# Performance work log

Measured on AMD Instinct MI355X. Metric: run time of the kernel, lower is better.

The kernel has to match this reference:

```python
import jax, jax.numpy as jnp
import numpy as np

B, S, D, E, H = 4, 2048, 1024, 8, 2048


def setup_inputs() -> dict:
    key = jax.random.key(0)
    ks = jax.random.split(key, 8)
    s_in = 1.0 / np.sqrt(D)   # torch Linear default init scale (uniform bound)
    s_hid = 1.0 / np.sqrt(H)
    return {
        "x": jax.random.normal(ks[0], (B, S, D), dtype=jnp.float32),
        "W1": jax.random.uniform(ks[1], (E, D, H), minval=-s_in, maxval=s_in, dtype=jnp.float32),
        "b1": jax.random.uniform(ks[2], (E, H), minval=-s_in, maxval=s_in, dtype=jnp.float32),
        "W2": jax.random.uniform(ks[3], (E, H, D), minval=-s_hid, maxval=s_hid, dtype=jnp.float32),
        "b2": jax.random.uniform(ks[4], (E, D), minval=-s_hid, maxval=s_hid, dtype=jnp.float32),
        "Wg": jax.random.uniform(ks[5], (D, E), minval=-s_in, maxval=s_in, dtype=jnp.float32),
        "bg": jax.random.uniform(ks[6], (E,), minval=-s_in, maxval=s_in, dtype=jnp.float32),
    }


def reference(x, W1, b1, W2, b2, Wg, bg):
    # All-experts dense MoE (eval mode: dropout is identity).
    # hidden: [B,S,E,H]
    h = jax.nn.relu(jnp.einsum("bsd,edh->bseh", x, W1) + b1)
    # expert outputs: [B,S,E,D]
    expert_out = jnp.einsum("bseh,ehd->bsed", h, W2) + b2
    # gate (raw linear, no softmax in original): [B,S,E]
    gate = jnp.einsum("bsd,de->bse", x, Wg) + bg
    # gate-weighted sum over experts -> [B,S,D]
    return jnp.einsum("bse,bsed->bsd", gate, expert_out)
```

## Files before the change

### kernel.cpp

```cpp
#include <hip/hip_runtime.h>

#define NTOK 8192
#define DDIM 1024
#define HDIM 2048
#define NEXP 8
#define GEXP 2
#define G1_NKT 16
#define G2_NKT 64

typedef unsigned short u16;
typedef short bf16x8 __attribute__((ext_vector_type(8)));
typedef float f32x4 __attribute__((ext_vector_type(4)));
typedef float float4_t __attribute__((ext_vector_type(4)));

__device__ __forceinline__ u16 f2bf(float f) {
  unsigned u = __float_as_uint(f);
  u += 0x7FFFu + ((u >> 16) & 1u);
  return (u16)(u >> 16);
}

#define GLOAD_LDS16(gp, lp)                                                     \
  __builtin_amdgcn_global_load_lds(                                             \
      (const __attribute__((address_space(1))) unsigned int*)(gp),              \
      (__attribute__((address_space(3))) unsigned int*)(lp), 16, 0, 0)

#define VMW(n) asm volatile("s_waitcnt vmcnt(" #n ")" ::: "memory")
#define ENTRYB()                                                                \
  { __builtin_amdgcn_s_barrier(); __builtin_amdgcn_sched_barrier(0); }

__global__ void k_prep(const float* __restrict__ x, const float* __restrict__ Wg,
                       const float* __restrict__ bg,
                       u16* __restrict__ xb, float* __restrict__ gate) {
  const int tok = (blockIdx.x * 256 + threadIdx.x) >> 6;
  const int lane = threadIdx.x & 63;
  const float* xr = x + (size_t)tok * DDIM;
  u16* xo = xb + (size_t)tok * DDIM;
  float s[NEXP];
#pragma unroll
  for (int e = 0; e < NEXP; ++e) s[e] = 0.f;
#pragma unroll
  for (int it = 0; it < 2; ++it) {
    const int d0 = lane * 8 + it * 512;
    float4_t v0 = *(const float4_t*)(xr + d0);
    float4_t v1 = *(const float4_t*)(xr + d0 + 4);
    union { bf16x8 v; u16 h[8]; } u;
    u.h[0] = f2bf(v0.x); u.h[1] = f2bf(v0.y); u.h[2] = f2bf(v0.z); u.h[3] = f2bf(v0.w);
    u.h[4] = f2bf(v1.x); u.h[5] = f2bf(v1.y); u.h[6] = f2bf(v1.z); u.h[7] = f2bf(v1.w);
    *(bf16x8*)(xo + d0) = u.v;
    float xv[8] = {v0.x, v0.y, v0.z, v0.w, v1.x, v1.y, v1.z, v1.w};
#pragma unroll
    for (int j = 0; j < 8; ++j) {
      const float4_t w0 = *(const float4_t*)(Wg + (size_t)(d0 + j) * NEXP);
      const float4_t w1 = *(const float4_t*)(Wg + (size_t)(d0 + j) * NEXP + 4);
      s[0] += xv[j] * w0.x; s[1] += xv[j] * w0.y;
      s[2] += xv[j] * w0.z; s[3] += xv[j] * w0.w;
      s[4] += xv[j] * w1.x; s[5] += xv[j] * w1.y;
      s[6] += xv[j] * w1.z; s[7] += xv[j] * w1.w;
    }
  }
#pragma unroll
  for (int off = 32; off; off >>= 1)
#pragma unroll
    for (int e = 0; e < NEXP; ++e) s[e] += __shfl_down(s[e], off);
  if (lane == 0) {
#pragma unroll
    for (int e = 0; e < NEXP; ++e) gate[(size_t)tok * NEXP + e] = s[e] + bg[e];
  }
}

__global__ void k_transpose(const float* __restrict__ in, u16* __restrict__ out,
                            int R, int C, size_t oexp, int orstride) {
  __shared__ float t[64][65];
  const int rb = blockIdx.x * 64, cb = blockIdx.y * 64;
  const float* pin = in + (size_t)blockIdx.z * R * C;
  u16* pout = out + (size_t)blockIdx.z * oexp;
  const int tid = threadIdx.x;
  {
    const int r = tid >> 4;
    const int c4 = (tid & 15) * 4;
#pragma unroll
    for (int i = 0; i < 4; ++i) {
      float4_t v = *(const float4_t*)(pin + (size_t)(rb + r + 16 * i) * C + cb + c4);
      t[r + 16 * i][c4 + 0] = v.x;
      t[r + 16 * i][c4 + 1] = v.y;
      t[r + 16 * i][c4 + 2] = v.z;
      t[r + 16 * i][c4 + 3] = v.w;
    }
  }
  __syncthreads();
  {
    const int oc = tid >> 3;
    const int r8 = (tid & 7) * 8;
#pragma unroll
    for (int jp = 0; jp < 2; ++jp) {
      const int ocol = oc + 32 * jp;
      union { bf16x8 v; u16 h[8]; } u;
#pragma unroll
      for (int k = 0; k < 8; ++k) u.h[k] = f2bf(t[r8 + k][ocol]);
      *(bf16x8*)(pout + (size_t)(cb + ocol) * orstride + rb + r8) = u.v;
    }
  }
}

__global__ __launch_bounds__(512, 2) void k_g1(
    const u16* __restrict__ A, const u16* __restrict__ Bt,
    const float* __restrict__ bias, const float* __restrict__ gate,
    int ebase, u16* __restrict__ Cout) {
  __shared__ __align__(16) u16 lds[65536];
  const int tid = threadIdx.x, lane = tid & 63, wid = tid >> 6;
  const int wm = wid >> 2, wn = wid & 3;
  const int wg = blockIdx.x;
  const int xcd = wg & 7, lo = wg >> 3;
  const int tm = (xcd >> 1) * 8 + (lo >> 3);
  const int tn = (xcd & 1) * 8 + (lo & 7);
  const int bm = tm * 256, bn = tn * 256;

  const int srow = tid >> 3;
  const int scol = ((tid & 7) ^ (srow & 7)) << 3;
  const u16* gA = A + (size_t)(bm + srow) * 1024 + scol;
  const u16* gB = Bt + (size_t)(bn + srow) * 1024 + scol;
  const int dofs = wid * 512;

  u16* aB0 = lds;          u16* bB0 = lds + 16384;
  u16* aB1 = lds + 32768;  u16* bB1 = lds + 49152;

  const int fr = lane & 15, fq = lane >> 4, xr = fr & 7;
  const int so0 = ((0 + fq) ^ xr) << 3;
  const int so1 = ((4 + fq) ^ xr) << 3;

  f32x4 acc[4][4][2] = {};
  bf16x8 av[4][2], bv[2][2];

#define G1_SA(dst, hh, ts)                                                      \
  { GLOAD_LDS16(gA + (size_t)((hh)*128     ) * 1024 + (size_t)(ts) * 64,        \
                (dst) + ((hh)*128     ) * 64 + dofs);                           \
    GLOAD_LDS16(gA + (size_t)((hh)*128 + 64) * 1024 + (size_t)(ts) * 64,        \
                (dst) + ((hh)*128 + 64) * 64 + dofs); }
#define G1_SB(dst, hh, ts)                                                      \
  { GLOAD_LDS16(gB + (size_t)((hh)*128     ) * 1024 + (size_t)(ts) * 64,        \
                (dst) + ((hh)*128     ) * 64 + dofs);                           \
    GLOAD_LDS16(gB + (size_t)((hh)*128 + 64) * 1024 + (size_t)(ts) * 64,        \
                (dst) + ((hh)*128 + 64) * 64 + dofs); }
#define RD_A(src, MH)                                                           \
  { _Pragma("unroll") for (int i_ = 0; i_ < 4; ++i_) {                          \
      const int rb_ = ((MH)*128 + wm * 64 + i_ * 16 + fr) << 6;                 \
      av[i_][0] = *(const bf16x8*)((src) + rb_ + so0);                          \
      av[i_][1] = *(const bf16x8*)((src) + rb_ + so1); } }
#define RD_B(src, NH)                                                           \
  { _Pragma("unroll") for (int n_ = 0; n_ < 2; ++n_) {                          \
      const int rb_ = ((NH)*128 + wn * 32 + n_ * 16 + fr) << 6;                 \
      bv[n_][0] = *(const bf16x8*)((src) + rb_ + so0);                          \
      bv[n_][1] = *(const bf16x8*)((src) + rb_ + so1); } }
#define MMA16(Q)                                                                \
  { __builtin_amdgcn_s_setprio(1);                                              \
    _Pragma("unroll") for (int i_ = 0; i_ < 4; ++i_)                            \
    _Pragma("unroll") for (int n_ = 0; n_ < 2; ++n_) {                          \
      acc[Q][i_][n_] = __builtin_amdgcn_mfma_f32_16x16x32_bf16(                 \
          av[i_][0], bv[n_][0], acc[Q][i_][n_], 0, 0, 0);                       \
      acc[Q][i_][n_] = __builtin_amdgcn_mfma_f32_16x16x32_bf16(                 \
          av[i_][1], bv[n_][1], acc[Q][i_][n_], 0, 0, 0); }                     \
    __builtin_amdgcn_s_setprio(0); }

  G1_SA(aB0, 0, 0); G1_SB(bB0, 0, 0); G1_SA(aB0, 1, 0); G1_SB(bB0, 1, 0);

  u16 *aC_ = aB0, *bC_ = bB0, *aN_ = aB1, *bN_ = bB1;

#pragma unroll 1
  for (int t = 0; t < G1_NKT; ++t) {
    const bool s1 = (t + 1 < G1_NKT);
    VMW(4); ENTRYB();
    RD_A(aC_, 0); RD_B(bC_, 0);
    if (s1) G1_SA(aN_, 0, t + 1);
    MMA16(0);
    if (s1) { VMW(4); } else { VMW(2); }
    ENTRYB();
    RD_A(aC_, 1);
    if (s1) G1_SB(bN_, 0, t + 1);
    MMA16(2);
    if (s1) { VMW(4); } else { VMW(0); }
    ENTRYB();
    RD_B(bC_, 1);
    if (s1) G1_SA(aN_, 1, t + 1);
    MMA16(3);
    RD_A(aC_, 0);
    if (s1) G1_SB(bN_, 1, t + 1);
    MMA16(1);
    u16* tp;
    tp = aC_; aC_ = aN_; aN_ = tp;
    tp = bC_; bC_ = bN_; bN_ = tp;
  }

#pragma unroll
  for (int q = 0; q < 4; ++q) {
    const int MH = q >> 1, NH = q & 1;
    const int cb0 = bn + NH * 128 + wn * 32;
    const int e = ebase + (cb0 >> 11);
    float bcol[2];
#pragma unroll
    for (int n = 0; n < 2; ++n) bcol[n] = bias[cb0 + n * 16 + fr];
#pragma unroll
    for (int i = 0; i < 4; ++i) {
#pragma unroll
      for (int j = 0; j < 4; ++j) {
        const int r = bm + MH * 128 + wm * 64 + i * 16 + fq * 4 + j;
        const float g = gate[(size_t)r * NEXP + e];
#pragma unroll
        for (int n = 0; n < 2; ++n) {
          float v = fmaxf(acc[q][i][n][j] + bcol[n], 0.f) * g;
          Cout[(size_t)r * (GEXP * HDIM) + cb0 + n * 16 + fr] = f2bf(v);
        }
      }
    }
  }
#undef G1_SA
#undef G1_SB
#undef RD_A
#undef RD_B
#undef MMA16
}

__global__ __launch_bounds__(512, 2) void k_g2(
    const u16* __restrict__ A, const u16* __restrict__ Bt,
    const float* __restrict__ bias, const float* __restrict__ gate,
    float* __restrict__ Cout, int accum) {
  __shared__ __align__(16) u16 lds[49152];
  const int tid = threadIdx.x, lane = tid & 63, wid = tid >> 6;
  const int wm = wid >> 2, wn = wid & 3;
  const int wg = blockIdx.x;
  const int xcd = wg & 7, lo = wg >> 3;
  const int tm = xcd * 8 + (lo >> 2);
  const int tn = lo & 3;
  const int bm = tm * 128, bn = tn * 256;

  const int srow = tid >> 3;
  const int scol = ((tid & 7) ^ (srow & 7)) << 3;
  const u16* gA = A + (size_t)(bm + srow) * (GEXP * HDIM) + scol;
  const u16* gB = Bt + (size_t)(bn + srow) * HDIM + scol;
  const int dofs = wid * 512;

  u16* aB0 = lds;          u16* bB0 = lds + 8192;
  u16* aB1 = lds + 24576;  u16* bB1 = lds + 32768;

  const int fr = lane & 15, fq = lane >> 4, xr = fr & 7;
  const int so0 = ((0 + fq) ^ xr) << 3;
  const int so1 = ((4 + fq) ^ xr) << 3;

  f32x4 acc[2][4][2] = {};
  bf16x8 av[4][2], bv[2][2];

#define G2_BOFF(ts) ((size_t)((ts) >> 5) * ((size_t)DDIM * HDIM) +              \
                     (size_t)((ts) & 31) * 64)
#define G2_SA(dst, ts)                                                          \
  { GLOAD_LDS16(gA + (size_t)(ts) * 64, (dst) + dofs);                          \
    GLOAD_LDS16(gA + (size_t)64 * (GEXP * HDIM) + (size_t)(ts) * 64,            \
                (dst) + 4096 + dofs); }
#define G2_SB(dst, hh, ts)                                                      \
  { GLOAD_LDS16(gB + (size_t)((hh)*128     ) * HDIM + G2_BOFF(ts),              \
                (dst) + ((hh)*128     ) * 64 + dofs);                           \
    GLOAD_LDS16(gB + (size_t)((hh)*128 + 64) * HDIM + G2_BOFF(ts),              \
                (dst) + ((hh)*128 + 64) * 64 + dofs); }
#define G2_RDA(src)                                                             \
  { _Pragma("unroll") for (int i_ = 0; i_ < 4; ++i_) {                          \
      const int rb_ = (wm * 64 + i_ * 16 + fr) << 6;                            \
      av[i_][0] = *(const bf16x8*)((src) + rb_ + so0);                          \
      av[i_][1] = *(const bf16x8*)((src) + rb_ + so1); } }
#define G2_RDB(src, NH)                                                         \
  { _Pragma("unroll") for (int n_ = 0; n_ < 2; ++n_) {                          \
      const int rb_ = ((NH)*128 + wn * 32 + n_ * 16 + fr) << 6;                 \
      bv[n_][0] = *(const bf16x8*)((src) + rb_ + so0);                          \
      bv[n_][1] = *(const bf16x8*)((src) + rb_ + so1); } }
#define G2_MMA(Q)                                                               \
  { __builtin_amdgcn_s_setprio(1);                                              \
    _Pragma("unroll") for (int i_ = 0; i_ < 4; ++i_)                            \
    _Pragma("unroll") for (int n_ = 0; n_ < 2; ++n_) {                          \
      acc[Q][i_][n_] = __builtin_amdgcn_mfma_f32_16x16x32_bf16(                 \
          av[i_][0], bv[n_][0], acc[Q][i_][n_], 0, 0, 0);                       \
      acc[Q][i_][n_] = __builtin_amdgcn_mfma_f32_16x16x32_bf16(                 \
          av[i_][1], bv[n_][1], acc[Q][i_][n_], 0, 0, 0); }                     \
    __builtin_amdgcn_s_setprio(0); }

  G2_SA(aB0, 0); G2_SB(bB0, 0, 0); G2_SB(bB0, 1, 0);

  u16 *aC_ = aB0, *bC_ = bB0, *aN_ = aB1, *bN_ = bB1;

#pragma unroll 1
  for (int t = 0; t < G2_NKT; ++t) {
    const bool s1 = (t + 1 < G2_NKT);
    VMW(2); ENTRYB();
    G2_RDA(aC_); G2_RDB(bC_, 0);
    if (s1) { G2_SA(aN_, t + 1); G2_SB(bN_, 0, t + 1); }
    G2_MMA(0);
    if (s1) { VMW(4); } else { VMW(0); }
    ENTRYB();
    G2_RDB(bC_, 1);
    if (s1) G2_SB(bN_, 1, t + 1);
    G2_MMA(1);
    u16* tp;
    tp = aC_; aC_ = aN_; aN_ = tp;
    tp = bC_; bC_ = bN_; bN_ = tp;
  }

  float b2c[2][2][NEXP];
  if (!accum) {
#pragma unroll
    for (int nh = 0; nh < 2; ++nh)
#pragma unroll
      for (int n = 0; n < 2; ++n)
#pragma unroll
        for (int e = 0; e < NEXP; ++e)
          b2c[nh][n][e] = bias[(size_t)e * DDIM + bn + nh * 128 + wn * 32 + n * 16 + fr];
  }
#pragma unroll
  for (int NH = 0; NH < 2; ++NH) {
    const int cb0 = bn + NH * 128 + wn * 32;
#pragma unroll
    for (int i = 0; i < 4; ++i) {
#pragma unroll
      for (int j = 0; j < 4; ++j) {
        const int r = bm + wm * 64 + i * 16 + fq * 4 + j;
        if (!accum) {
          float g8[NEXP];
#pragma unroll
          for (int e = 0; e < NEXP; ++e) g8[e] = gate[(size_t)r * NEXP + e];
#pragma unroll
          for (int n = 0; n < 2; ++n) {
            float v = acc[NH][i][n][j];
#pragma unroll
            for (int e = 0; e < NEXP; ++e) v += g8[e] * b2c[NH][n][e];
            Cout[(size_t)r * DDIM + cb0 + n * 16 + fr] = v;
          }
        } else {
#pragma unroll
          for (int n = 0; n < 2; ++n) {
            const size_t idx = (size_t)r * DDIM + cb0 + n * 16 + fr;
            Cout[idx] += acc[NH][i][n][j];
          }
        }
      }
    }
  }
#undef G2_BOFF
#undef G2_SA
#undef G2_SB
#undef G2_RDA
#undef G2_RDB
#undef G2_MMA
}

extern "C" void kernel_launch(void* const* d_in, const int* in_sizes, int n_in,
                              void* d_out, int out_size, void* d_ws, size_t ws_size,
                              hipStream_t stream) {
  (void)in_sizes; (void)n_in; (void)out_size;
  const float* x  = (const float*)d_in[0];
  const float* W1 = (const float*)d_in[1];
  const float* b1 = (const float*)d_in[2];
  const float* W2 = (const float*)d_in[3];
  const float* b2 = (const float*)d_in[4];
  const float* Wg = (const float*)d_in[5];
  const float* bg = (const float*)d_in[6];
  float* out = (float*)d_out;

  size_t o_xb   = 0;
  size_t o_w1t  = o_xb  + (size_t)NTOK * DDIM * 2;
  size_t o_w2t  = o_w1t + (size_t)NEXP * HDIM * DDIM * 2;
  size_t o_gate = o_w2t + (size_t)NEXP * DDIM * HDIM * 2;
  size_t o_h    = o_gate + (size_t)NTOK * NEXP * 4;
  size_t need   = o_h   + (size_t)NTOK * GEXP * HDIM * 2;
  if (ws_size < need) return;

  u16*   xb   = (u16*)((char*)d_ws + o_xb);
  u16*   W1t  = (u16*)((char*)d_ws + o_w1t);
  u16*   W2t  = (u16*)((char*)d_ws + o_w2t);
  float* gate = (float*)((char*)d_ws + o_gate);
  u16*   hbuf = (u16*)((char*)d_ws + o_h);

  k_prep<<<NTOK / 4, 256, 0, stream>>>(x, Wg, bg, xb, gate);
  dim3 g1(DDIM / 64, HDIM / 64, NEXP);
  k_transpose<<<g1, 256, 0, stream>>>(W1, W1t, DDIM, HDIM, (size_t)HDIM * DDIM, DDIM);
  dim3 g2(HDIM / 64, DDIM / 64, NEXP);
  k_transpose<<<g2, 256, 0, stream>>>(W2, W2t, HDIM, DDIM, (size_t)DDIM * HDIM, HDIM);

  const int Ng = GEXP * HDIM;
  for (int g = 0; g < NEXP / GEXP; ++g) {
    k_g1<<<512, 512, 0, stream>>>(
        xb, W1t + (size_t)g * Ng * DDIM,
        b1 + (size_t)g * Ng, gate, g * GEXP, hbuf);
    k_g2<<<256, 512, 0, stream>>>(
        hbuf, W2t + (size_t)g * GEXP * DDIM * HDIM,
        b2, gate, out, g > 0);
  }
}
```

Baseline: 630.8 us.

## Process four experts per group and split LDS reads per k-half

Expert grouping goes from 2 to 4 when the workspace allows it. This halves the number of g1/g2 launch pairs, halves the read-modify-write passes over the fp32 output, and doubles the K-loop length in g2. The block-to-tile mapping in g1 is parameterized so the larger grid still maps onto the 8 XCDs. LDS fragment reads and MFMA ordering are also split by k-half, so the first half's MFMAs can start before the second half's reads finish. The cost is a larger hidden-activation buffer, with a fallback to groups of 2 when the workspace is too small.

```diff
diff --git a/kernel.cpp b/kernel.cpp
--- a/kernel.cpp
+++ b/kernel.cpp
@@ -4,9 +4,7 @@
 #define DDIM 1024
 #define HDIM 2048
 #define NEXP 8
-#define GEXP 2
 #define G1_NKT 16
-#define G2_NKT 64
 
 typedef unsigned short u16;
 typedef short bf16x8 __attribute__((ext_vector_type(8)));
@@ -105,14 +103,15 @@
 __global__ __launch_bounds__(512, 2) void k_g1(
     const u16* __restrict__ A, const u16* __restrict__ Bt,
     const float* __restrict__ bias, const float* __restrict__ gate,
-    int ebase, u16* __restrict__ Cout) {
+    int ebase, u16* __restrict__ Cout, int KW, int ca, int cgcols) {
   __shared__ __align__(16) u16 lds[65536];
   const int tid = threadIdx.x, lane = tid & 63, wid = tid >> 6;
   const int wm = wid >> 2, wn = wid & 3;
   const int wg = blockIdx.x;
   const int xcd = wg & 7, lo = wg >> 3;
-  const int tm = (xcd >> 1) * 8 + (lo >> 3);
-  const int tn = (xcd & 1) * 8 + (lo & 7);
+  const int cr = xcd / cgcols, cc = xcd % cgcols;
+  const int tm = cr * ca + (lo >> 3);
+  const int tn = cc * 8 + (lo & 7);
   const int bm = tm * 256, bn = tn * 256;
 
   const int srow = tid >> 3;
@@ -141,24 +140,21 @@
                 (dst) + ((hh)*128     ) * 64 + dofs);                           \
     GLOAD_LDS16(gB + (size_t)((hh)*128 + 64) * 1024 + (size_t)(ts) * 64,        \
                 (dst) + ((hh)*128 + 64) * 64 + dofs); }
-#define RD_A(src, MH)                                                           \
+#define RD_A_K(src, MH, KK)                                                     \
   { _Pragma("unroll") for (int i_ = 0; i_ < 4; ++i_) {                          \
       const int rb_ = ((MH)*128 + wm * 64 + i_ * 16 + fr) << 6;                 \
-      av[i_][0] = *(const bf16x8*)((src) + rb_ + so0);                          \
-      av[i_][1] = *(const bf16x8*)((src) + rb_ + so1); } }
-#define RD_B(src, NH)                                                           \
+      av[i_][KK] = *(const bf16x8*)((src) + rb_ + ((KK) ? so1 : so0)); } }
+#define RD_B_K(src, NH, KK)                                                     \
   { _Pragma("unroll") for (int n_ = 0; n_ < 2; ++n_) {                          \
       const int rb_ = ((NH)*128 + wn * 32 + n_ * 16 + fr) << 6;                 \
-      bv[n_][0] = *(const bf16x8*)((src) + rb_ + so0);                          \
-      bv[n_][1] = *(const bf16x8*)((src) + rb_ + so1); } }
+      bv[n_][KK] = *(const bf16x8*)((src) + rb_ + ((KK) ? so1 : so0)); } }
 #define MMA16(Q)                                                                \
   { __builtin_amdgcn_s_setprio(1);                                              \
+    _Pragma("unroll") for (int k_ = 0; k_ < 2; ++k_)                            \
     _Pragma("unroll") for (int i_ = 0; i_ < 4; ++i_)                            \
-    _Pragma("unroll") for (int n_ = 0; n_ < 2; ++n_) {                          \
+    _Pragma("unroll") for (int n_ = 0; n_ < 2; ++n_)                            \
       acc[Q][i_][n_] = __builtin_amdgcn_mfma_f32_16x16x32_bf16(                 \
-          av[i_][0], bv[n_][0], acc[Q][i_][n_], 0, 0, 0);                       \
-      acc[Q][i_][n_] = __builtin_amdgcn_mfma_f32_16x16x32_bf16(                 \
-          av[i_][1], bv[n_][1], acc[Q][i_][n_], 0, 0, 0); }                     \
+          av[i_][k_], bv[n_][k_], acc[Q][i_][n_], 0, 0, 0);                     \
     __builtin_amdgcn_s_setprio(0); }
 
   G1_SA(aB0, 0, 0); G1_SB(bB0, 0, 0); G1_SA(aB0, 1, 0); G1_SB(bB0, 1, 0);
@@ -169,20 +165,21 @@
   for (int t = 0; t < G1_NKT; ++t) {
     const bool s1 = (t + 1 < G1_NKT);
     VMW(4); ENTRYB();
-    RD_A(aC_, 0); RD_B(bC_, 0);
+    RD_A_K(aC_, 0, 0); RD_B_K(bC_, 0, 0);
+    RD_A_K(aC_, 0, 1); RD_B_K(bC_, 0, 1);
     if (s1) G1_SA(aN_, 0, t + 1);
     MMA16(0);
     if (s1) { VMW(4); } else { VMW(2); }
     ENTRYB();
-    RD_A(aC_, 1);
+    RD_A_K(aC_, 1, 0); RD_A_K(aC_, 1, 1);
     if (s1) G1_SB(bN_, 0, t + 1);
     MMA16(2);
     if (s1) { VMW(4); } else { VMW(0); }
     ENTRYB();
-    RD_B(bC_, 1);
+    RD_B_K(bC_, 1, 0); RD_B_K(bC_, 1, 1);
     if (s1) G1_SA(aN_, 1, t + 1);
     MMA16(3);
-    RD_A(aC_, 0);
+    RD_A_K(aC_, 0, 0); RD_A_K(aC_, 0, 1);
     if (s1) G1_SB(bN_, 1, t + 1);
     MMA16(1);
     u16* tp;
@@ -207,22 +204,22 @@
 #pragma unroll
         for (int n = 0; n < 2; ++n) {
           float v = fmaxf(acc[q][i][n][j] + bcol[n], 0.f) * g;
-          Cout[(size_t)r * (GEXP * HDIM) + cb0 + n * 16 + fr] = f2bf(v);
+          Cout[(size_t)r * KW + cb0 + n * 16 + fr] = f2bf(v);
         }
       }
     }
   }
 #undef G1_SA
 #undef G1_SB
-#undef RD_A
-#undef RD_B
+#undef RD_A_K
+#undef RD_B_K
 #undef MMA16
 }
 
 __global__ __launch_bounds__(512, 2) void k_g2(
     const u16* __restrict__ A, const u16* __restrict__ Bt,
     const float* __restrict__ bias, const float* __restrict__ gate,
-    float* __restrict__ Cout, int accum) {
+    float* __restrict__ Cout, int accum, int KW, int nk) {
   __shared__ __align__(16) u16 lds[49152];
   const int tid = threadIdx.x, lane = tid & 63, wid = tid >> 6;
   const int wm = wid >> 2, wn = wid & 3;
@@ -234,7 +231,7 @@
 
   const int srow = tid >> 3;
   const int scol = ((tid & 7) ^ (srow & 7)) << 3;
-  const u16* gA = A + (size_t)(bm + srow) * (GEXP * HDIM) + scol;
+  const u16* gA = A + (size_t)(bm + srow) * KW + scol;
   const u16* gB = Bt + (size_t)(bn + srow) * HDIM + scol;
   const int dofs = wid * 512;
 
@@ -252,31 +249,28 @@
                      (size_t)((ts) & 31) * 64)
 #define G2_SA(dst, ts)                                                          \
   { GLOAD_LDS16(gA + (size_t)(ts) * 64, (dst) + dofs);                          \
-    GLOAD_LDS16(gA + (size_t)64 * (GEXP * HDIM) + (size_t)(ts) * 64,            \
+    GLOAD_LDS16(gA + (size_t)64 * KW + (size_t)(ts) * 64,                       \
                 (dst) + 4096 + dofs); }
 #define G2_SB(dst, hh, ts)                                                      \
   { GLOAD_LDS16(gB + (size_t)((hh)*128     ) * HDIM + G2_BOFF(ts),              \
                 (dst) + ((hh)*128     ) * 64 + dofs);                           \
     GLOAD_LDS16(gB + (size_t)((hh)*128 + 64) * HDIM + G2_BOFF(ts),              \
                 (dst) + ((hh)*128 + 64) * 64 + dofs); }
-#define G2_RDA(src)                                                             \
+#define G2_RDA_K(src, KK)                                                       \
   { _Pragma("unroll") for (int i_ = 0; i_ < 4; ++i_) {                          \
       const int rb_ = (wm * 64 + i_ * 16 + fr) << 6;                            \
-      av[i_][0] = *(const bf16x8*)((src) + rb_ + so0);                          \
-      av[i_][1] = *(const bf16x8*)((src) + rb_ + so1); } }
-#define G2_RDB(src, NH)                                                         \
+      av[i_][KK] = *(const bf16x8*)((src) + rb_ + ((KK) ? so1 : so0)); } }
+#define G2_RDB_K(src, NH, KK)                                                   \
   { _Pragma("unroll") for (int n_ = 0; n_ < 2; ++n_) {                          \
       const int rb_ = ((NH)*128 + wn * 32 + n_ * 16 + fr) << 6;                 \
-      bv[n_][0] = *(const bf16x8*)((src) + rb_ + so0);                          \
-      bv[n_][1] = *(const bf16x8*)((src) + rb_ + so1); } }
+      bv[n_][KK] = *(const bf16x8*)((src) + rb_ + ((KK) ? so1 : so0)); } }
 #define G2_MMA(Q)                                                               \
   { __builtin_amdgcn_s_setprio(1);                                              \
+    _Pragma("unroll") for (int k_ = 0; k_ < 2; ++k_)                            \
     _Pragma("unroll") for (int i_ = 0; i_ < 4; ++i_)                            \
-    _Pragma("unroll") for (int n_ = 0; n_ < 2; ++n_) {                          \
+    _Pragma("unroll") for (int n_ = 0; n_ < 2; ++n_)                            \
       acc[Q][i_][n_] = __builtin_amdgcn_mfma_f32_16x16x32_bf16(                 \
-          av[i_][0], bv[n_][0], acc[Q][i_][n_], 0, 0, 0);                       \
-      acc[Q][i_][n_] = __builtin_amdgcn_mfma_f32_16x16x32_bf16(                 \
-          av[i_][1], bv[n_][1], acc[Q][i_][n_], 0, 0, 0); }                     \
+          av[i_][k_], bv[n_][k_], acc[Q][i_][n_], 0, 0, 0);                     \
     __builtin_amdgcn_s_setprio(0); }
 
   G2_SA(aB0, 0); G2_SB(bB0, 0, 0); G2_SB(bB0, 1, 0);
@@ -284,15 +278,16 @@
   u16 *aC_ = aB0, *bC_ = bB0, *aN_ = aB1, *bN_ = bB1;
 
 #pragma unroll 1
-  for (int t = 0; t < G2_NKT; ++t) {
-    const bool s1 = (t + 1 < G2_NKT);
+  for (int t = 0; t < nk; ++t) {
+    const bool s1 = (t + 1 < nk);
     VMW(2); ENTRYB();
-    G2_RDA(aC_); G2_RDB(bC_, 0);
+    G2_RDA_K(aC_, 0); G2_RDB_K(bC_, 0, 0);
+    G2_RDA_K(aC_, 1); G2_RDB_K(bC_, 0, 1);
     if (s1) { G2_SA(aN_, t + 1); G2_SB(bN_, 0, t + 1); }
     G2_MMA(0);
     if (s1) { VMW(4); } else { VMW(0); }
     ENTRYB();
-    G2_RDB(bC_, 1);
+    G2_RDB_K(bC_, 1, 0); G2_RDB_K(bC_, 1, 1);
     if (s1) G2_SB(bN_, 1, t + 1);
     G2_MMA(1);
     u16* tp;
@@ -342,8 +337,8 @@
 #undef G2_BOFF
 #undef G2_SA
 #undef G2_SB
-#undef G2_RDA
-#undef G2_RDB
+#undef G2_RDA_K
+#undef G2_RDB_K
 #undef G2_MMA
 }
 
@@ -365,8 +360,10 @@
   size_t o_w2t  = o_w1t + (size_t)NEXP * HDIM * DDIM * 2;
   size_t o_gate = o_w2t + (size_t)NEXP * DDIM * HDIM * 2;
   size_t o_h    = o_gate + (size_t)NTOK * NEXP * 4;
-  size_t need   = o_h   + (size_t)NTOK * GEXP * HDIM * 2;
-  if (ws_size < need) return;
+
+  int G = 4;
+  if (o_h + (size_t)NTOK * G * HDIM * 2 > ws_size) G = 2;
+  if (o_h + (size_t)NTOK * G * HDIM * 2 > ws_size) return;
 
   u16*   xb   = (u16*)((char*)d_ws + o_xb);
   u16*   W1t  = (u16*)((char*)d_ws + o_w1t);
@@ -380,13 +377,15 @@
   dim3 g2(HDIM / 64, DDIM / 64, NEXP);
   k_transpose<<<g2, 256, 0, stream>>>(W2, W2t, HDIM, DDIM, (size_t)DDIM * HDIM, HDIM);
 
-  const int Ng = GEXP * HDIM;
-  for (int g = 0; g < NEXP / GEXP; ++g) {
-    k_g1<<<512, 512, 0, stream>>>(
-        xb, W1t + (size_t)g * Ng * DDIM,
-        b1 + (size_t)g * Ng, gate, g * GEXP, hbuf);
+  const int KW = G * HDIM;
+  const int ca1 = (G == 4) ? 16 : 8;
+  const int cg1 = (G == 4) ? 4 : 2;
+  for (int g = 0; g < NEXP / G; ++g) {
+    k_g1<<<(NTOK / 256) * (KW / 256), 512, 0, stream>>>(
+        xb, W1t + (size_t)g * KW * DDIM,
+        b1 + (size_t)g * KW, gate, g * G, hbuf, KW, ca1, cg1);
     k_g2<<<256, 512, 0, stream>>>(
-        hbuf, W2t + (size_t)g * GEXP * DDIM * HDIM,
-        b2, gate, out, g > 0);
-  }
-}
+        hbuf, W2t + (size_t)g * G * DDIM * HDIM,
+        b2, gate, out, g > 0, KW, KW / 64);
+  }
+}
```

Result: faster. 589.5 us (-6.5%).
